# Performance work log

Hardware: AMD Instinct MI355X
Metric: run time of the kernel (lower is better)

The kernel has to match this reference:

```python
import jax, jax.numpy as jnp
import numpy as np

B, S, HID = 1, 4096, 1024
H, KV, D = 16, 4, 64           # heads, kv heads, head_dim
N_REP = H // KV
WINDOW = 512
EPS = 1e-5
ROPE_THETA = 1e6


def _rope_tables(seq_len, dim, theta):
    inv_freq = 1.0 / (theta ** (np.arange(0, dim, 2, dtype=np.float32) / dim))
    t = np.arange(seq_len, dtype=np.float32)
    freqs = np.outer(t, inv_freq)                      # [S, D/2]
    emb = np.concatenate([freqs, freqs], axis=-1)      # [S, D]
    return jnp.asarray(np.cos(emb)), jnp.asarray(np.sin(emb))


def setup_inputs() -> dict:
    key = jax.random.key(0)
    ks = jax.random.split(key, 7)
    cos, sin = _rope_tables(S, D, ROPE_THETA)
    return {
        "x": jax.random.normal(ks[0], (B, S, HID), jnp.float32),
        "cos": cos,
        "sin": sin,
        "wq": jax.random.normal(ks[1], (H * D, HID), jnp.float32) * (HID ** -0.5),
        "wk": jax.random.normal(ks[2], (KV * D, HID), jnp.float32) * (HID ** -0.5),
        "wv": jax.random.normal(ks[3], (KV * D, HID), jnp.float32) * (HID ** -0.5),
        "wo": jax.random.normal(ks[4], (HID, H * D), jnp.float32) * (HID ** -0.5),
        "q_norm_w": jnp.ones((D,), jnp.float32),
        "k_norm_w": jnp.ones((D,), jnp.float32),
        "sinks": jax.random.normal(ks[5], (H,), jnp.float32),
    }


def _rms_norm(v, w):
    return v * jax.lax.rsqrt(jnp.mean(v * v, axis=-1, keepdims=True) + EPS) * w


def _rotate_half(v):
    h = v.shape[-1] // 2
    return jnp.concatenate([-v[..., h:], v[..., :h]], axis=-1)


def reference(x, cos, sin, wq, wk, wv, wo, q_norm_w, k_norm_w, sinks):
    b, s, _ = x.shape
    q = (x @ wq.T).reshape(b, s, H, D)
    k = (x @ wk.T).reshape(b, s, KV, D)
    v = (x @ wv.T).reshape(b, s, KV, D)
    q = _rms_norm(q, q_norm_w)
    k = _rms_norm(k, k_norm_w)
    c = cos[:, None, :]  # [s,1,d] broadcast over heads
    sn = sin[:, None, :]
    q = q * c + _rotate_half(q) * sn
    k = k * c + _rotate_half(k) * sn
    # GQA: repeat kv heads
    k = jnp.repeat(k, N_REP, axis=2)  # [b,s,H,D]
    v = jnp.repeat(v, N_REP, axis=2)
    scores = jnp.einsum("bqhd,bkhd->bhqk", q, k) / np.sqrt(D)  # [b,H,s,s]
    i = jnp.arange(s)[:, None]
    j = jnp.arange(s)[None, :]
    allowed = (j <= i) & (j > i - WINDOW)  # causal + sliding window
    scores = jnp.where(allowed, scores, -jnp.inf)
    # append per-head learned sink logit, softmax in fp32, then drop sink col
    sink = jnp.broadcast_to(sinks.reshape(1, H, 1, 1), (b, H, s, 1))
    attn = jax.nn.softmax(jnp.concatenate([scores, sink], axis=-1).astype(jnp.float32), axis=-1)
    attn = attn[..., :-1].astype(q.dtype)
    out = jnp.einsum("bhqk,bkhd->bqhd", attn, v).reshape(b, s, H * D)
    return out @ wo.T
```

## Files before the change

### kernel.cpp

```cpp
#include <hip/hip_runtime.h>
#include <hip/hip_bf16.h>
#include <stdint.h>

#define S_LEN   4096
#define HIDDEN  1024
#define NHEAD   16
#define NKV     4
#define HD      64
#define WINDOW  512
#define L2E     1.4426950408889634f
#define QSCALE  (0.125f * L2E)

using short8 = __attribute__((ext_vector_type(8))) short;
using f32x4  = __attribute__((ext_vector_type(4))) float;

__device__ __forceinline__ uint16_t f2bf(float f) {
  uint32_t u = __builtin_bit_cast(uint32_t, f);
  u += 0x7fffu + ((u >> 16) & 1u);
  return (uint16_t)(u >> 16);
}
__device__ __forceinline__ uint16_t f2bf_rn(float f) {
  uint32_t u = __builtin_bit_cast(uint32_t, f);
  return (uint16_t)((u + 0x8000u) >> 16);
}
__device__ __forceinline__ uint32_t pk2(float a, float b) {
  return (uint32_t)f2bf_rn(a) | ((uint32_t)f2bf_rn(b) << 16);
}

__device__ __forceinline__ void gld_lds16(void* lds, const void* g) {
  __builtin_amdgcn_global_load_lds(
      (const __attribute__((address_space(1))) char*)g,
      (__attribute__((address_space(3))) char*)lds, 16, 0, 0);
}

__global__ __launch_bounds__(256) void k_tobf16(
    const float* __restrict__ x, const float* __restrict__ wq,
    const float* __restrict__ wk, const float* __restrict__ wv,
    const float* __restrict__ wo,
    uint16_t* __restrict__ xb, uint16_t* __restrict__ wqkvb,
    uint16_t* __restrict__ wob) {
  int i = blockIdx.x * 256 + threadIdx.x;
  const float4* src; uint16_t* dst; int off;
  if (i < 1048576)      { src = (const float4*)x;  dst = xb;                off = i; }
  else if (i < 1310720) { src = (const float4*)wq; dst = wqkvb;             off = i - 1048576; }
  else if (i < 1376256) { src = (const float4*)wk; dst = wqkvb + 1024*1024; off = i - 1310720; }
  else if (i < 1441792) { src = (const float4*)wv; dst = wqkvb + 1280*1024; off = i - 1376256; }
  else                  { src = (const float4*)wo; dst = wob;               off = i - 1441792; }
  float4 v = src[off];
  ushort4 o = { f2bf(v.x), f2bf(v.y), f2bf(v.z), f2bf(v.w) };
  *(ushort4*)(dst + (size_t)off * 4) = o;
}

__global__ __launch_bounds__(256) void k_gemm_qkv(
    const uint16_t* __restrict__ A, const uint16_t* __restrict__ B,
    const float* __restrict__ cosb, const float* __restrict__ sinb,
    const float* __restrict__ qw, const float* __restrict__ kw,
    uint16_t* __restrict__ qout, uint16_t* __restrict__ kout,
    uint16_t* __restrict__ vtout) {
  __shared__ uint16_t As[64 * 64];
  __shared__ uint16_t Bs[128 * 64];
  const int K = 1024;
  const int t = threadIdx.x;
  const int lane = t & 63, w = t >> 6;
  const int wr = w >> 1, wc = w & 1;
  const int l16 = lane & 15, lg = lane >> 4;
  const int bm = blockIdx.x, bn = blockIdx.y;
  const uint16_t* Ab = A + (size_t)bm * 64 * K;
  const uint16_t* Bb = B + (size_t)bn * 128 * K;
  f32x4 acc[2][4] = {};
  for (int k0 = 0; k0 < K; k0 += 64) {
    __syncthreads();
    {
      int row = t >> 3, c8 = (t & 7) << 3;
      gld_lds16(&As[t * 8], Ab + (size_t)row * K + k0 + c8);
      int t2 = t + 256, row2 = t2 >> 3, c82 = (t2 & 7) << 3;
      gld_lds16(&As[t2 * 8], Ab + (size_t)row2 * K + k0 + c82);
    }
#pragma unroll
    for (int it = 0; it < 4; ++it) {
      int idx = it * 256 + t;
      int row = idx >> 3, c8 = (idx & 7) << 3;
      gld_lds16(&Bs[idx * 8], Bb + (size_t)row * K + k0 + c8);
    }
    __syncthreads();
#pragma unroll
    for (int kk = 0; kk < 2; ++kk) {
      short8 af[2], bq[4];
#pragma unroll
      for (int i = 0; i < 2; ++i)
        af[i] = *(const short8*)&As[(wr * 32 + i * 16 + l16) * 64 + kk * 32 + lg * 8];
#pragma unroll
      for (int j = 0; j < 4; ++j)
        bq[j] = *(const short8*)&Bs[(wc * 64 + j * 16 + l16) * 64 + kk * 32 + lg * 8];
#pragma unroll
      for (int i = 0; i < 2; ++i)
#pragma unroll
        for (int j = 0; j < 4; ++j)
          acc[i][j] = __builtin_amdgcn_mfma_f32_16x16x32_bf16(af[i], bq[j], acc[i][j], 0, 0, 0);
    }
  }

  const int hg = bn * 2 + wc;
  if (hg >= 20) {
    const int kvh = hg - 20;
#pragma unroll
    for (int i = 0; i < 2; ++i) {
      int row0 = bm * 64 + wr * 32 + i * 16 + lg * 4;
#pragma unroll
      for (int j = 0; j < 4; ++j) {
        int d = j * 16 + l16;
        ushort4 o = { f2bf(acc[i][j][0]), f2bf(acc[i][j][1]),
                      f2bf(acc[i][j][2]), f2bf(acc[i][j][3]) };
        *(ushort4*)(vtout + (size_t)(kvh * 64 + d) * S_LEN + row0) = o;
      }
    }
    return;
  }
  const float* nw = (hg < 16) ? qw : kw;
  float wgt[4];
#pragma unroll
  for (int j = 0; j < 4; ++j) wgt[j] = nw[j * 16 + l16];
#pragma unroll
  for (int i = 0; i < 2; ++i) {
    int row0 = bm * 64 + wr * 32 + i * 16 + lg * 4;
    float qn[4][4];
#pragma unroll
    for (int r = 0; r < 4; ++r) {
      float ss = acc[i][0][r] * acc[i][0][r] + acc[i][1][r] * acc[i][1][r]
               + acc[i][2][r] * acc[i][2][r] + acc[i][3][r] * acc[i][3][r];
      ss += __shfl_xor(ss, 1);
      ss += __shfl_xor(ss, 2);
      ss += __shfl_xor(ss, 4);
      ss += __shfl_xor(ss, 8);
      float inv = rsqrtf(ss * (1.0f / 64.0f) + 1e-5f);
#pragma unroll
      for (int j = 0; j < 4; ++j) qn[j][r] = acc[i][j][r] * inv * wgt[j];
    }
#pragma unroll
    for (int j = 0; j < 4; ++j) {
      int d = j * 16 + l16;
#pragma unroll
      for (int r = 0; r < 4; ++r) {
        int row = row0 + r;
        float rot = (j < 2) ? -qn[j + 2][r] : qn[j - 2][r];
        float o = qn[j][r] * cosb[row * 64 + d] + rot * sinb[row * 64 + d];
        if (hg < 16)
          qout[(size_t)row * HIDDEN + hg * 64 + d] = f2bf(o * QSCALE);
        else
          kout[((size_t)(hg - 16) * S_LEN + row) * 64 + d] = f2bf(o);
      }
    }
  }
}

__global__ __launch_bounds__(256) void k_gemm_bf16(
    const uint16_t* __restrict__ A, const uint16_t* __restrict__ B,
    float* __restrict__ C, int N, int K) {
  __shared__ uint16_t As[64 * 64];
  __shared__ uint16_t Bs[128 * 64];
  const int t = threadIdx.x;
  const int lane = t & 63, w = t >> 6;
  const int wr = w >> 1, wc = w & 1;
  const int l16 = lane & 15, lg = lane >> 4;
  const int bm = blockIdx.x, bn = blockIdx.y;
  const uint16_t* Ab = A + (size_t)bm * 64 * K;
  const uint16_t* Bb = B + (size_t)bn * 128 * K;
  f32x4 acc[2][4] = {};
  for (int k0 = 0; k0 < K; k0 += 64) {
    __syncthreads();
    {
      int row = t >> 3, c8 = (t & 7) << 3;
      gld_lds16(&As[t * 8], Ab + (size_t)row * K + k0 + c8);
      int t2 = t + 256, row2 = t2 >> 3, c82 = (t2 & 7) << 3;
      gld_lds16(&As[t2 * 8], Ab + (size_t)row2 * K + k0 + c82);
    }
#pragma unroll
    for (int it = 0; it < 4; ++it) {
      int idx = it * 256 + t;
      int row = idx >> 3, c8 = (idx & 7) << 3;
      gld_lds16(&Bs[idx * 8], Bb + (size_t)row * K + k0 + c8);
    }
    __syncthreads();
#pragma unroll
    for (int kk = 0; kk < 2; ++kk) {
      short8 af[2], bq[4];
#pragma unroll
      for (int i = 0; i < 2; ++i)
        af[i] = *(const short8*)&As[(wr * 32 + i * 16 + l16) * 64 + kk * 32 + lg * 8];
#pragma unroll
      for (int j = 0; j < 4; ++j)
        bq[j] = *(const short8*)&Bs[(wc * 64 + j * 16 + l16) * 64 + kk * 32 + lg * 8];
#pragma unroll
      for (int i = 0; i < 2; ++i)
#pragma unroll
        for (int j = 0; j < 4; ++j)
          acc[i][j] = __builtin_amdgcn_mfma_f32_16x16x32_bf16(af[i], bq[j], acc[i][j], 0, 0, 0);
    }
  }
#pragma unroll
  for (int i = 0; i < 2; ++i) {
    int row0 = bm * 64 + wr * 32 + i * 16 + lg * 4;
#pragma unroll
    for (int j = 0; j < 4; ++j) {
      int col = bn * 128 + wc * 64 + j * 16 + l16;
#pragma unroll
      for (int r = 0; r < 4; ++r)
        C[(size_t)(row0 + r) * N + col] = acc[i][j][r];
    }
  }
}

__global__ __launch_bounds__(512) void k_attn(
    const uint16_t* __restrict__ qb,
    const uint16_t* __restrict__ kb,
    const uint16_t* __restrict__ vtb,
    const float* __restrict__ sinks,
    uint16_t* __restrict__ ao) {
  __shared__ uint16_t Kl[64][72];
  __shared__ uint16_t Vl[64][72];
  __shared__ uint16_t Pl[8][16][72];
  const int q0 = (63 - blockIdx.x) * 64;
  const int hp = blockIdx.y;
  const int kvh = hp >> 1;
  const int t = threadIdx.x;
  const int lane = t & 63, w = t >> 6;
  const int h = kvh * 4 + (hp & 1) * 2 + (w >> 2);
  const int wq = w & 3;
  const int l16 = lane & 15, lg = lane >> 4;
  const int qrow = q0 + wq * 16 + l16;

  short8 bq0, bq1;
  {
    const uint16_t* qp = qb + (size_t)qrow * HIDDEN + h * 64 + lg * 8;
    bq0 = *(const short8*)qp;
    bq1 = *(const short8*)(qp + 32);
  }
  float lsum = 0.f;
  f32x4 acc[4] = {};

  int kstart = q0 - WINDOW;
  if (kstart < 0) kstart = 0;
  for (int k0 = kstart; k0 <= q0; k0 += 64) {
    __syncthreads();
    {
      int row = t >> 3, c8 = (t & 7) << 3;
      *(short8*)&Kl[row][c8] =
          *(const short8*)(kb + ((size_t)kvh * S_LEN + k0 + row) * 64 + c8);
      *(short8*)&Vl[row][c8] =
          *(const short8*)(vtb + ((size_t)kvh * 64 + row) * S_LEN + k0 + c8);
    }
    __syncthreads();

    f32x4 st[4] = {};
#pragma unroll
    for (int c = 0; c < 4; ++c) {
      short8 ak0 = *(const short8*)&Kl[c * 16 + l16][lg * 8];
      short8 ak1 = *(const short8*)&Kl[c * 16 + l16][32 + lg * 8];
      st[c] = __builtin_amdgcn_mfma_f32_16x16x32_bf16(ak0, bq0, st[c], 0, 0, 0);
      st[c] = __builtin_amdgcn_mfma_f32_16x16x32_bf16(ak1, bq1, st[c], 0, 0, 0);
    }

    float p[4][4];
    if (k0 == q0 || k0 == q0 - WINDOW) {
#pragma unroll
      for (int c = 0; c < 4; ++c) {
        int keyb = k0 + c * 16 + lg * 4;
#pragma unroll
        for (int r = 0; r < 4; ++r) {
          int key = keyb + r;
          bool ok = (key <= qrow) && (key + WINDOW > qrow);
          p[c][r] = ok ? exp2f(st[c][r]) : 0.f;
        }
      }
    } else {
#pragma unroll
      for (int c = 0; c < 4; ++c)
#pragma unroll
        for (int r = 0; r < 4; ++r)
          p[c][r] = exp2f(st[c][r]);
    }
#pragma unroll
    for (int c = 0; c < 4; ++c)
      lsum += (p[c][0] + p[c][1]) + (p[c][2] + p[c][3]);

#pragma unroll
    for (int c = 0; c < 4; ++c) {
      uint2 pw = { pk2(p[c][0], p[c][1]), pk2(p[c][2], p[c][3]) };
      *(uint2*)&Pl[w][l16][c * 16 + lg * 4] = pw;
    }
    asm volatile("s_waitcnt lgkmcnt(0)" ::: "memory");
    short8 pa0 = *(const short8*)&Pl[w][l16][lg * 8];
    short8 pa1 = *(const short8*)&Pl[w][l16][32 + lg * 8];
#pragma unroll
    for (int dt = 0; dt < 4; ++dt) {
      short8 bv0 = *(const short8*)&Vl[dt * 16 + l16][lg * 8];
      short8 bv1 = *(const short8*)&Vl[dt * 16 + l16][32 + lg * 8];
      acc[dt] = __builtin_amdgcn_mfma_f32_16x16x32_bf16(pa0, bv0, acc[dt], 0, 0, 0);
      acc[dt] = __builtin_amdgcn_mfma_f32_16x16x32_bf16(pa1, bv1, acc[dt], 0, 0, 0);
    }
  }

  lsum += __shfl_xor(lsum, 16);
  lsum += __shfl_xor(lsum, 32);
  float sk = exp2f(sinks[h] * L2E);
  float inv = 1.0f / (lsum + sk);
#pragma unroll
  for (int r = 0; r < 4; ++r) {
    float rd = __shfl(inv, lg * 4 + r);
    int row = q0 + wq * 16 + lg * 4 + r;
#pragma unroll
    for (int dt = 0; dt < 4; ++dt)
      ao[(size_t)row * HIDDEN + h * 64 + dt * 16 + l16] = f2bf(acc[dt][r] * rd);
  }
}

extern "C" void kernel_launch(void* const* d_in, const int* in_sizes, int n_in,
                              void* d_out, int out_size, void* d_ws, size_t ws_size,
                              hipStream_t stream) {
  const float* x     = (const float*)d_in[0];
  const float* cosb  = (const float*)d_in[1];
  const float* sinb  = (const float*)d_in[2];
  const float* wq    = (const float*)d_in[3];
  const float* wk    = (const float*)d_in[4];
  const float* wv    = (const float*)d_in[5];
  const float* wo    = (const float*)d_in[6];
  const float* qnw   = (const float*)d_in[7];
  const float* knw   = (const float*)d_in[8];
  const float* sinks = (const float*)d_in[9];
  float* out = (float*)d_out;

  char* ws = (char*)d_ws;
  uint16_t* xb    = (uint16_t*)(ws);
  uint16_t* wqkvb = (uint16_t*)(ws + (8ll  << 20));
  uint16_t* wob   = (uint16_t*)(ws + (11ll << 20));
  uint16_t* qsc   = (uint16_t*)(ws + (13ll << 20));
  uint16_t* kbf   = (uint16_t*)(ws + (21ll << 20));
  uint16_t* vtb   = (uint16_t*)(ws + (23ll << 20));
  uint16_t* aob   = (uint16_t*)(ws + (25ll << 20));

  k_tobf16  <<<6656, 256, 0, stream>>>(x, wq, wk, wv, wo, xb, wqkvb, wob);
  k_gemm_qkv<<<dim3(64, 12), 256, 0, stream>>>(xb, wqkvb, cosb, sinb, qnw, knw,
                                               qsc, kbf, vtb);
  k_attn    <<<dim3(64, 8), 512, 0, stream>>>(qsc, kbf, vtb, sinks, aob);
  k_gemm_bf16<<<dim3(64, 8), 256, 0, stream>>>(aob, wob, out, 1024, 1024);
}
```

Measured before the change: 83.10 us.

## Rewrite attention with 32x32 MFMA, direct global K/V loads, register P shuffles

The attention kernel now has each wave compute a 32-query tile using 32x32x16 MFMA instructions. K and V are read straight from global memory instead of being staged in LDS, so the per-tile __syncthreads go away. P is rearranged across lanes with shuffles rather than an LDS round trip. Blocks shrink to 256 threads and the block index is remapped so consecutive blocks go to different head pairs. This removes barrier and LDS traffic, but K/V reuse now depends on the cache and each wave issues more global loads.

Result: slower. 96.72 us (+16.4%).

```diff
diff --git a/kernel.cpp b/kernel.cpp
--- a/kernel.cpp
+++ b/kernel.cpp
@@ -13,6 +13,7 @@
 
 using short8 = __attribute__((ext_vector_type(8))) short;
 using f32x4  = __attribute__((ext_vector_type(4))) float;
+using f32x16 = __attribute__((ext_vector_type(16))) float;
 
 __device__ __forceinline__ uint16_t f2bf(float f) {
   uint32_t u = __builtin_bit_cast(uint32_t, f);
@@ -210,107 +211,97 @@
   }
 }
 
-__global__ __launch_bounds__(512) void k_attn(
+__global__ __launch_bounds__(256) void k_attn(
     const uint16_t* __restrict__ qb,
     const uint16_t* __restrict__ kb,
     const uint16_t* __restrict__ vtb,
     const float* __restrict__ sinks,
     uint16_t* __restrict__ ao) {
-  __shared__ uint16_t Kl[64][72];
-  __shared__ uint16_t Vl[64][72];
-  __shared__ uint16_t Pl[8][16][72];
-  const int q0 = (63 - blockIdx.x) * 64;
-  const int hp = blockIdx.y;
-  const int kvh = hp >> 1;
   const int t = threadIdx.x;
   const int lane = t & 63, w = t >> 6;
-  const int h = kvh * 4 + (hp & 1) * 2 + (w >> 2);
-  const int wq = w & 3;
-  const int l16 = lane & 15, lg = lane >> 4;
-  const int qrow = q0 + wq * 16 + l16;
-
-  short8 bq0, bq1;
+  const int linear = blockIdx.x + 64 * blockIdx.y;
+  const int lid = (linear & 7) * 64 + (linear >> 3);
+  const int q0 = (63 - (lid & 63)) * 64;
+  const int hp = lid >> 6;
+  const int kvh = hp >> 1;
+  const int h = kvh * 4 + (hp & 1) * 2 + (w >> 1);
+  const int qbase = q0 + (w & 1) * 32;
+  const int l32 = lane & 31, hi = lane >> 5;
+  const int qrow = qbase + l32;
+
+  short8 bq[4];
   {
-    const uint16_t* qp = qb + (size_t)qrow * HIDDEN + h * 64 + lg * 8;
-    bq0 = *(const short8*)qp;
-    bq1 = *(const short8*)(qp + 32);
-  }
+    const uint16_t* qp = qb + (size_t)qrow * HIDDEN + h * 64 + hi * 8;
+    bq[0] = *(const short8*)(qp);
+    bq[1] = *(const short8*)(qp + 16);
+    bq[2] = *(const short8*)(qp + 32);
+    bq[3] = *(const short8*)(qp + 48);
+  }
+  const uint16_t* kbase = kb + (size_t)kvh * S_LEN * 64;
+  const uint16_t* vbase = vtb + (size_t)kvh * 64 * S_LEN;
+
+  f32x16 acc0 = {}, acc1 = {};
   float lsum = 0.f;
-  f32x4 acc[4] = {};
-
   int kstart = q0 - WINDOW;
   if (kstart < 0) kstart = 0;
+
   for (int k0 = kstart; k0 <= q0; k0 += 64) {
-    __syncthreads();
-    {
-      int row = t >> 3, c8 = (t & 7) << 3;
-      *(short8*)&Kl[row][c8] =
-          *(const short8*)(kb + ((size_t)kvh * S_LEN + k0 + row) * 64 + c8);
-      *(short8*)&Vl[row][c8] =
-          *(const short8*)(vtb + ((size_t)kvh * 64 + row) * S_LEN + k0 + c8);
-    }
-    __syncthreads();
-
-    f32x4 st[4] = {};
-#pragma unroll
-    for (int c = 0; c < 4; ++c) {
-      short8 ak0 = *(const short8*)&Kl[c * 16 + l16][lg * 8];
-      short8 ak1 = *(const short8*)&Kl[c * 16 + l16][32 + lg * 8];
-      st[c] = __builtin_amdgcn_mfma_f32_16x16x32_bf16(ak0, bq0, st[c], 0, 0, 0);
-      st[c] = __builtin_amdgcn_mfma_f32_16x16x32_bf16(ak1, bq1, st[c], 0, 0, 0);
-    }
-
-    float p[4][4];
-    if (k0 == q0 || k0 == q0 - WINDOW) {
-#pragma unroll
-      for (int c = 0; c < 4; ++c) {
-        int keyb = k0 + c * 16 + lg * 4;
-#pragma unroll
-        for (int r = 0; r < 4; ++r) {
-          int key = keyb + r;
+    const bool edge = (k0 == q0) || (k0 == q0 - WINDOW);
+    const uint16_t* kt = kbase + (size_t)(k0 + l32) * 64 + hi * 8;
+#pragma unroll
+    for (int c = 0; c < 2; ++c) {
+      f32x16 st = {};
+#pragma unroll
+      for (int s = 0; s < 4; ++s) {
+        short8 ak = *(const short8*)(kt + c * 32 * 64 + s * 16);
+        st = __builtin_amdgcn_mfma_f32_32x32x16_bf16(ak, bq[s], st, 0, 0, 0);
+      }
+      float pp[16];
+      if (edge) {
+#pragma unroll
+        for (int r = 0; r < 16; ++r) {
+          int key = k0 + c * 32 + 4 * hi + (r & 3) + 8 * (r >> 2);
           bool ok = (key <= qrow) && (key + WINDOW > qrow);
-          p[c][r] = ok ? exp2f(st[c][r]) : 0.f;
+          pp[r] = ok ? exp2f(st[r]) : 0.f;
         }
-      }
-    } else {
-#pragma unroll
-      for (int c = 0; c < 4; ++c)
-#pragma unroll
-        for (int r = 0; r < 4; ++r)
-          p[c][r] = exp2f(st[c][r]);
-    }
-#pragma unroll
-    for (int c = 0; c < 4; ++c)
-      lsum += (p[c][0] + p[c][1]) + (p[c][2] + p[c][3]);
-
-#pragma unroll
-    for (int c = 0; c < 4; ++c) {
-      uint2 pw = { pk2(p[c][0], p[c][1]), pk2(p[c][2], p[c][3]) };
-      *(uint2*)&Pl[w][l16][c * 16 + lg * 4] = pw;
-    }
-    asm volatile("s_waitcnt lgkmcnt(0)" ::: "memory");
-    short8 pa0 = *(const short8*)&Pl[w][l16][lg * 8];
-    short8 pa1 = *(const short8*)&Pl[w][l16][32 + lg * 8];
-#pragma unroll
-    for (int dt = 0; dt < 4; ++dt) {
-      short8 bv0 = *(const short8*)&Vl[dt * 16 + l16][lg * 8];
-      short8 bv1 = *(const short8*)&Vl[dt * 16 + l16][32 + lg * 8];
-      acc[dt] = __builtin_amdgcn_mfma_f32_16x16x32_bf16(pa0, bv0, acc[dt], 0, 0, 0);
-      acc[dt] = __builtin_amdgcn_mfma_f32_16x16x32_bf16(pa1, bv1, acc[dt], 0, 0, 0);
-    }
-  }
-
-  lsum += __shfl_xor(lsum, 16);
+      } else {
+#pragma unroll
+        for (int r = 0; r < 16; ++r) pp[r] = exp2f(st[r]);
+      }
+#pragma unroll
+      for (int r = 0; r < 16; ++r) lsum += pp[r];
+      uint32_t wvp[8];
+#pragma unroll
+      for (int i = 0; i < 8; ++i) wvp[i] = pk2(pp[2 * i], pp[2 * i + 1]);
+#pragma unroll
+      for (int half = 0; half < 2; ++half) {
+        uint32_t x0 = wvp[half * 4 + 0], x1 = wvp[half * 4 + 1];
+        uint32_t x2 = wvp[half * 4 + 2], x3 = wvp[half * 4 + 3];
+        uint32_t p0 = (uint32_t)__shfl_xor((int)x0, 32);
+        uint32_t p1 = (uint32_t)__shfl_xor((int)x1, 32);
+        uint32_t p2 = (uint32_t)__shfl_xor((int)x2, 32);
+        uint32_t p3 = (uint32_t)__shfl_xor((int)x3, 32);
+        uint4 au = { hi ? p2 : x0, hi ? p3 : x1, hi ? x2 : p0, hi ? x3 : p1 };
+        short8 pa = __builtin_bit_cast(short8, au);
+        const uint16_t* vt = vbase + (size_t)l32 * S_LEN
+                           + k0 + c * 32 + half * 16 + hi * 8;
+        short8 bv0 = *(const short8*)(vt);
+        short8 bv1 = *(const short8*)(vt + 32 * S_LEN);
+        acc0 = __builtin_amdgcn_mfma_f32_32x32x16_bf16(pa, bv0, acc0, 0, 0, 0);
+        acc1 = __builtin_amdgcn_mfma_f32_32x32x16_bf16(pa, bv1, acc1, 0, 0, 0);
+      }
+    }
+  }
+
   lsum += __shfl_xor(lsum, 32);
-  float sk = exp2f(sinks[h] * L2E);
-  float inv = 1.0f / (lsum + sk);
-#pragma unroll
-  for (int r = 0; r < 4; ++r) {
-    float rd = __shfl(inv, lg * 4 + r);
-    int row = q0 + wq * 16 + lg * 4 + r;
-#pragma unroll
-    for (int dt = 0; dt < 4; ++dt)
-      ao[(size_t)row * HIDDEN + h * 64 + dt * 16 + l16] = f2bf(acc[dt][r] * rd);
+  float inv = 1.0f / (lsum + exp2f(sinks[h] * L2E));
+#pragma unroll
+  for (int r = 0; r < 16; ++r) {
+    int rloc = (r & 3) + 8 * (r >> 2) + 4 * hi;
+    float rd = __shfl(inv, rloc);
+    size_t base = (size_t)(qbase + rloc) * HIDDEN + h * 64 + l32;
+    ao[base]      = f2bf(acc0[r] * rd);
+    ao[base + 32] = f2bf(acc1[r] * rd);
   }
 }
 
@@ -341,6 +332,6 @@
   k_tobf16  <<<6656, 256, 0, stream>>>(x, wq, wk, wv, wo, xb, wqkvb, wob);
   k_gemm_qkv<<<dim3(64, 12), 256, 0, stream>>>(xb, wqkvb, cosb, sinb, qnw, knw,
                                                qsc, kbf, vtb);
-  k_attn    <<<dim3(64, 8), 512, 0, stream>>>(qsc, kbf, vtb, sinks, aob);
+  k_attn    <<<dim3(64, 8), 256, 0, stream>>>(qsc, kbf, vtb, sinks, aob);
   k_gemm_bf16<<<dim3(64, 8), 256, 0, stream>>>(aob, wob, out, 1024, 1024);
 }
```
